# Kernel optimization log

Hardware: AMD Instinct MI355X
Metric: run time of the kernel (lower is better)

Reference implementation:

```python
import jax, jax.numpy as jnp
import numpy as np

B, T, D, W, H = 64, 512, 768, 255, 8
DH = D // H

def layernorm(x, g, b, eps=1e-5):
    m = jnp.mean(x, axis=-1, keepdims=True)
    v = jnp.mean((x - m) ** 2, axis=-1, keepdims=True)
    return (x - m) * jax.lax.rsqrt(v + eps) * g + b

def setup_inputs() -> dict:
    key = jax.random.key(0)
    ks = list(jax.random.split(key, 12))
    p = lambda k, shape, s=0.02: (jax.random.normal(k, shape, jnp.float32) * s)
    # words_ids: -100 at CLS/SEP, each word spans 2 subtokens -> 255 words/row
    wi = np.full((B, T), -100, dtype=np.int32)
    pos = np.arange(1, T - 1)
    wi[:, 1:T - 1] = (pos - 1) // 2
    return {
        'output_bert': jax.random.normal(ks[0], (B, T, D), jnp.float32),
        'words_ids': jnp.asarray(wi),
        'Wq': p(ks[1], (D, D)), 'bq': jnp.zeros((D,), jnp.float32),
        'Wk': p(ks[2], (D, D)), 'bk': jnp.zeros((D,), jnp.float32),
        'Wv': p(ks[3], (D, D)), 'bv': jnp.zeros((D,), jnp.float32),
        'Wo': p(ks[4], (D, D)), 'bo': jnp.zeros((D,), jnp.float32),
        'ln1_g': jnp.ones((D,), jnp.float32), 'ln1_b': jnp.zeros((D,), jnp.float32),
        'W1f': p(ks[5], (D, 4 * D)), 'b1f': jnp.zeros((4 * D,), jnp.float32),
        'W2f': p(ks[6], (4 * D, D)), 'b2f': jnp.zeros((D,), jnp.float32),
        'ln2_g': jnp.ones((D,), jnp.float32), 'ln2_b': jnp.zeros((D,), jnp.float32),
        'ng': jnp.ones((D,), jnp.float32), 'nb': jnp.zeros((D,), jnp.float32),
        'lin_w': p(ks[7], (D, 2)), 'lin_b': jnp.zeros((2,), jnp.float32),
    }

def reference(output_bert, words_ids, Wq, bq, Wk, bk, Wv, bv, Wo, bo,
              ln1_g, ln1_b, W1f, b1f, W2f, b2f, ln2_g, ln2_b, ng, nb, lin_w, lin_b):
    Bsz = output_bert.shape[0]
    # --- first-subtoken gather: first token position of each word id ---
    hits = words_ids[:, None, :] == jnp.arange(W)[None, :, None]   # [B, W, T]
    first_idx = jnp.argmax(hits, axis=-1)                           # [B, W]
    feat = jnp.take_along_axis(output_bert, first_idx[..., None], axis=1)  # [B, W, D]
    # --- transformer encoder layer (post-norm, relu FFN) ---
    q = (feat @ Wq + bq).reshape(Bsz, W, H, DH)
    k = (feat @ Wk + bk).reshape(Bsz, W, H, DH)
    v = (feat @ Wv + bv).reshape(Bsz, W, H, DH)
    scores = jnp.einsum('bqhd,bkhd->bhqk', q, k) * (1.0 / np.sqrt(DH))
    attn = jax.nn.softmax(scores, axis=-1)
    ctx = jnp.einsum('bhqk,bkhd->bqhd', attn, v).reshape(Bsz, W, D)
    x = layernorm(feat + ctx @ Wo + bo, ln1_g, ln1_b)
    ff = jax.nn.relu(x @ W1f + b1f) @ W2f + b2f
    x = layernorm(x + ff, ln2_g, ln2_b)
    # --- final LayerNorm + Linear + softmax + argmax path ---
    x = layernorm(x, ng, nb)
    logits = x @ lin_w + lin_b
    ner_prob = jax.nn.softmax(logits, axis=-1)
    path = jnp.argmax(ner_prob, axis=-1)
    return ner_prob, path
```

## Files before the change

### kernel.cpp

```cpp
#include <hip/hip_runtime.h>
#include <cmath>

#define Bsz 64
#define Tt  512
#define Dd  768
#define Wn  255
#define Hh  8
#define DHd 96
#define NROWS (Bsz*Wn)

typedef _Float16 half_t;
typedef _Float16 f16x8 __attribute__((ext_vector_type(8)));
typedef _Float16 f16x4 __attribute__((ext_vector_type(4)));
typedef float f32x4 __attribute__((ext_vector_type(4)));

#define OFF_QKV 0
#define OFF_WO  5308416
#define OFF_W1  7077888
#define OFF_W2  14155776
#define SLOTH 25165824
__device__ __align__(16) half_t g_w16[21233664];

__device__ __forceinline__ void gload16(const half_t* g, half_t* l) {
    __builtin_amdgcn_global_load_lds((const __attribute__((address_space(1))) void*)g,
                                     (__attribute__((address_space(3))) void*)l, 16, 0, 0);
}


__global__ void k_init_fi(int* fi) {
    int i = blockIdx.x * 256 + threadIdx.x;
    if (i < Bsz * Wn) fi[i] = 0x7fffffff;
}

__global__ void k_scan(const int* __restrict__ wid, int* __restrict__ fi) {
    int i = blockIdx.x * 256 + threadIdx.x;
    if (i >= Bsz * Tt) return;
    int b = i / Tt, t = i % Tt;
    int w = wid[i];
    if (w >= 0 && w < Wn) atomicMin(&fi[b * Wn + w], t);
}

__global__ void k_bcat(const float* __restrict__ bq, const float* __restrict__ bk,
                       const float* __restrict__ bv, float* __restrict__ o) {
    int i = blockIdx.x * 256 + threadIdx.x;
    if (i < 768) o[i] = bq[i];
    else if (i < 1536) o[i] = bk[i - 768];
    else if (i < 2304) o[i] = bv[i - 1536];
}

__global__ void k_gather(const float4* __restrict__ ob, const int* __restrict__ fi,
                         half_t* __restrict__ f16) {
    int i = blockIdx.x * 256 + threadIdx.x;
    if (i >= NROWS * 192) return;
    int r = i / 192, c = i % 192;
    int b = r / Wn;
    int idx = fi[r];
    if (idx == 0x7fffffff) idx = 0;
    float4 v = ob[((size_t)b * Tt + idx) * 192 + c];
    float a0 = v.x * 16.f, a1 = v.y * 16.f, a2 = v.z * 16.f, a3 = v.w * 16.f;
    half_t h0 = (half_t)a0, h1 = (half_t)a1, h2 = (half_t)a2, h3 = (half_t)a3;
    f16x4 hv = {h0, h1, h2, h3};
    f16x4 lv = {(half_t)(a0 - (float)h0), (half_t)(a1 - (float)h1),
                (half_t)(a2 - (float)h2), (half_t)(a3 - (float)h3)};
    size_t off = (size_t)r * 1536 + c * 4;
    *(f16x4*)&f16[off] = hv;
    *(f16x4*)&f16[off + 768] = lv;
}


__global__ void k_wsplit(const float* __restrict__ Wm, int K, int N,
                         size_t obase, int Kseg, size_t cstride) {
    __shared__ float sm[32][33];
    const int tx = threadIdx.x, ty = threadIdx.y;
    const int n0 = blockIdx.x * 32, k0 = blockIdx.y * 32;
    #pragma unroll
    for (int r = 0; r < 4; ++r)
        sm[ty + r * 8][tx] = Wm[(size_t)(k0 + ty + r * 8) * N + n0 + tx];
    __syncthreads();
    #pragma unroll
    for (int r = 0; r < 4; ++r) {
        float v = 64.f * sm[tx][ty + r * 8];
        half_t hi = (half_t)v;
        half_t lo = (half_t)(v - (float)hi);
        int k = k0 + tx;
        int n = n0 + ty + r * 8;
        int c = k / Kseg, kk = k - c * Kseg;
        half_t* o = g_w16 + obase + (size_t)c * cstride + (size_t)n * (3 * Kseg) + kk;
        o[0] = hi; o[Kseg] = hi; o[2 * Kseg] = lo;
    }
}


__device__ __forceinline__ void stage_b(const half_t* B, int Kp3, int col0,
                                        int t, int c, half_t* dst, int tid) {
    int gc = col0 + c * 64 + (tid >> 3);
    int sj = (tid & 7) ^ ((tid >> 3) & 7);
    gload16(B + (size_t)gc * Kp3 + (size_t)t * 64 + sj * 8,
            dst + 16384 + c * 4096 + (tid >> 6) * 512);
}

__device__ __forceinline__ void stage_a0(const half_t* Ap, int lda, int row0, int M,
                                         int kk, int c, half_t* dst, int tid) {
    int gr = row0 + c * 64 + (tid >> 3); if (gr > M - 1) gr = M - 1;
    int sj = (tid & 7) ^ ((tid >> 3) & 7);
    gload16(Ap + (size_t)gr * lda + kk + sj * 8, dst + c * 4096 + (tid >> 6) * 512);
}

__device__ __forceinline__ void stage_a1(const half_t* qcb, int row0, int M,
                                         int kk, int soff, int c, half_t* dst, int tid) {
    int gr = row0 + c * 64 + (tid >> 3); if (gr > M - 1) gr = M - 1;
    int sj = (tid & 7) ^ ((tid >> 3) & 7);
    int k = kk + sj * 8;
    int h = k / 96, d = k - h * 96;
    int b = gr / 255, wl = gr - b * 255;
    gload16(qcb + ((size_t)(b * 8 + h) * 256 + wl) * 192 + d + soff,
            dst + c * 4096 + (tid >> 6) * 512);
}

template<int MODE, int AMODE>
__global__ __launch_bounds__(512, 2) void k_gemm256(
    const half_t* __restrict__ Ah, const half_t* __restrict__ Al, int lda,
    size_t boff, const float* __restrict__ bias,
    const void* res, void* out0, void* out1,
    int M, int N, int K) {
    __shared__ half_t sm[2][32768];
    const int tid = threadIdx.x;
    const int w = tid >> 6, l = tid & 63;
    const int wm = w >> 2, wn = w & 3;
    const int fr = l & 15, q4 = l >> 4;
    const int ck0 = (q4 * 8) ^ ((fr & 7) << 3);
    const int ck1 = ck0 ^ 32;
    const half_t* Bsrc = g_w16 + boff;
    const int Kp3 = 3 * K, NT = Kp3 >> 6;

    int lin = blockIdx.y * gridDim.x + blockIdx.x;
    int nwg = gridDim.x * gridDim.y;
    int wg = (lin & 7) * (nwg >> 3) + (lin >> 3);
    int by = wg / gridDim.x, bx = wg - by * gridDim.x;
    const int row0 = by * 256, col0 = bx * 256;

    f32x4 acc[8][4];
    #pragma unroll
    for (int m = 0; m < 8; ++m)
        #pragma unroll
        for (int n = 0; n < 4; ++n) acc[m][n] = (f32x4){0.f, 0.f, 0.f, 0.f};

    {
        half_t* d0 = &sm[0][0];
        stage_b(Bsrc, Kp3, col0, 0, 0, d0, tid);
        stage_b(Bsrc, Kp3, col0, 0, 1, d0, tid);
        stage_b(Bsrc, Kp3, col0, 0, 2, d0, tid);
        stage_b(Bsrc, Kp3, col0, 0, 3, d0, tid);
        if (AMODE == 0) {
            stage_a0(Ah, lda, row0, M, 0, 0, d0, tid);
            stage_a0(Ah, lda, row0, M, 0, 2, d0, tid);
            stage_a0(Ah, lda, row0, M, 0, 1, d0, tid);
            stage_a0(Ah, lda, row0, M, 0, 3, d0, tid);
        } else {
            stage_a1(Ah, row0, M, 0, 0, 0, d0, tid);
            stage_a1(Ah, row0, M, 0, 0, 2, d0, tid);
            stage_a1(Ah, row0, M, 0, 0, 1, d0, tid);
            stage_a1(Ah, row0, M, 0, 0, 3, d0, tid);
        }
    }
    asm volatile("s_waitcnt vmcnt(2)" ::: "memory");
    __builtin_amdgcn_s_barrier();
    asm volatile("" ::: "memory");

    for (int t = 0; t < NT; ++t) {
        const int p = t & 1;
        half_t* nxtb = &sm[p ^ 1][0];
        const half_t* pA = &sm[p][0] + wm * 8192;
        const half_t* pB = &sm[p][0] + 16384 + wn * 4096;
        const bool pf = (t + 1) < NT;
        const int kn = (t + 1) << 6;
        const int seg = (kn >= 2 * K) ? 2 : ((kn >= K) ? 1 : 0);
        const int kkn = kn - seg * K;
        const half_t* An = (seg == 1) ? Al : Ah;
        const int soff = (seg == 1) ? 96 : 0;

        f16x8 b0[4], b1[4], a0[4], a1[4];
        #pragma unroll
        for (int n = 0; n < 4; ++n) {
            b0[n] = *(const f16x8*)&pB[n * 1024 + fr * 64 + ck0];
            b1[n] = *(const f16x8*)&pB[n * 1024 + fr * 64 + ck1];
        }
        #pragma unroll
        for (int m = 0; m < 4; ++m) {
            a0[m] = *(const f16x8*)&pA[m * 1024 + fr * 64 + ck0];
            a1[m] = *(const f16x8*)&pA[m * 1024 + fr * 64 + ck1];
        }
        if (pf) {
            stage_b(Bsrc, Kp3, col0, t + 1, 0, nxtb, tid);
            stage_b(Bsrc, Kp3, col0, t + 1, 1, nxtb, tid);
            stage_b(Bsrc, Kp3, col0, t + 1, 2, nxtb, tid);
            stage_b(Bsrc, Kp3, col0, t + 1, 3, nxtb, tid);
        }
        __builtin_amdgcn_s_setprio(1);
        #pragma unroll
        for (int m = 0; m < 4; ++m)
            #pragma unroll
            for (int n = 0; n < 4; ++n) {
                acc[m][n] = __builtin_amdgcn_mfma_f32_16x16x32_f16(a0[m], b0[n], acc[m][n], 0, 0, 0);
                acc[m][n] = __builtin_amdgcn_mfma_f32_16x16x32_f16(a1[m], b1[n], acc[m][n], 0, 0, 0);
            }
        __builtin_amdgcn_s_setprio(0);
        if (pf) asm volatile("s_waitcnt vmcnt(4)" ::: "memory");
        else    asm volatile("s_waitcnt vmcnt(0)" ::: "memory");
        __builtin_amdgcn_s_barrier();
        asm volatile("" ::: "memory");

        #pragma unroll
        for (int m = 0; m < 4; ++m) {
            a0[m] = *(const f16x8*)&pA[4096 + m * 1024 + fr * 64 + ck0];
            a1[m] = *(const f16x8*)&pA[4096 + m * 1024 + fr * 64 + ck1];
        }
        if (pf) {
            if (AMODE == 0) {
                stage_a0(An, lda, row0, M, kkn, 0, nxtb, tid);
                stage_a0(An, lda, row0, M, kkn, 2, nxtb, tid);
                stage_a0(An, lda, row0, M, kkn, 1, nxtb, tid);
                stage_a0(An, lda, row0, M, kkn, 3, nxtb, tid);
            } else {
                stage_a1(Ah, row0, M, kkn, soff, 0, nxtb, tid);
                stage_a1(Ah, row0, M, kkn, soff, 2, nxtb, tid);
                stage_a1(Ah, row0, M, kkn, soff, 1, nxtb, tid);
                stage_a1(Ah, row0, M, kkn, soff, 3, nxtb, tid);
            }
        }
        __builtin_amdgcn_s_setprio(1);
        #pragma unroll
        for (int m = 0; m < 4; ++m)
            #pragma unroll
            for (int n = 0; n < 4; ++n) {
                acc[4 + m][n] = __builtin_amdgcn_mfma_f32_16x16x32_f16(a0[m], b0[n], acc[4 + m][n], 0, 0, 0);
                acc[4 + m][n] = __builtin_amdgcn_mfma_f32_16x16x32_f16(a1[m], b1[n], acc[4 + m][n], 0, 0, 0);
            }
        __builtin_amdgcn_s_setprio(0);
        if (pf) {
            asm volatile("s_waitcnt vmcnt(2)" ::: "memory");
            __builtin_amdgcn_s_barrier();
            asm volatile("" ::: "memory");
        }
    }

    const float dsc = 1.0f / 1024.0f;
    #pragma unroll
    for (int m = 0; m < 8; ++m) {
        #pragma unroll
        for (int r = 0; r < 4; ++r) {
            const int row = row0 + wm * 128 + m * 16 + q4 * 4 + r;
            if (row >= M) continue;
            #pragma unroll
            for (int n = 0; n < 4; ++n) {
                const int col = col0 + wn * 64 + n * 16 + fr;
                float vv = acc[m][n][r] * dsc;
                if (MODE != 4) vv += bias[col];
                if (MODE == 5) {
                    int part = col / 768, cc = col - part * 768;
                    int h = cc / 96, d = cc - h * 96;
                    int b = row / 255, wl = row - b * 255;
                    float t16 = vv * 16.f;
                    half_t hi = (half_t)t16;
                    half_t lo = (half_t)(t16 - (float)hi);
                    half_t* dstp = (half_t*)out0 + (size_t)part * SLOTH;
                    size_t o = ((size_t)(b * 8 + h) * 256 + wl) * 192 + d;
                    dstp[o] = hi; dstp[o + 96] = lo;
                } else if (MODE == 1) {
                    const half_t* rp = (const half_t*)res;
                    vv += ((float)rp[(size_t)row * 1536 + col] +
                           (float)rp[(size_t)row * 1536 + 768 + col]) * 0.0625f;
                    ((float*)out0)[(size_t)row * N + col] = vv;
                } else if (MODE == 2) {
                    vv = fmaxf(vv, 0.f);
                    float t16 = vv * 16.f;
                    half_t hi = (half_t)t16;
                    ((half_t*)out0)[(size_t)row * N + col] = hi;
                    ((half_t*)out1)[(size_t)row * N + col] = (half_t)(t16 - (float)hi);
                } else if (MODE == 3) {
                    vv += ((const float*)res)[(size_t)row * N + col];
                    ((float*)out0)[(size_t)row * N + col] = vv;
                } else {
                    float* op = (float*)out0 + (size_t)row * N + col;
                    *op += vv;
                }
            }
        }
    }
}


__global__ __launch_bounds__(256, 2) void k_attn2(half_t* __restrict__ qc,
                                                  const half_t* __restrict__ kk16,
                                                  const half_t* __restrict__ vv16) {
    __shared__ half_t sK[64][200];
    __shared__ half_t sVT[192][72];
    __shared__ float  sP[4][16][68];
    const int tid = threadIdx.x;
    const int w = tid >> 6, l = tid & 63;
    const int lr = l & 15, lc = l >> 4;
    const size_t base = (size_t)blockIdx.x * 49152;
    const float ssc = 0.10206207261596575f / 256.0f;

    for (int pass = 0; pass < 2; ++pass) {
        f32x4 O[2][6];
        float mrow[2][4], lrow[2][4];
        #pragma unroll
        for (int qs = 0; qs < 2; ++qs) {
            #pragma unroll
            for (int dn = 0; dn < 6; ++dn) O[qs][dn] = (f32x4){0.f, 0.f, 0.f, 0.f};
            #pragma unroll
            for (int r = 0; r < 4; ++r) { mrow[qs][r] = -3e38f; lrow[qs][r] = 0.f; }
        }
        for (int kt = 0; kt < 4; ++kt) {
            __syncthreads();
            #pragma unroll
            for (int c = 0; c < 6; ++c) {
                int ch = w + c * 4;
                *(f16x8*)&sK[l][ch * 8] =
                    *(const f16x8*)(kk16 + base + (size_t)(kt * 64 + l) * 192 + ch * 8);
            }
            #pragma unroll
            for (int c = 0; c < 6; ++c) {
                int ch = w + c * 4;
                f16x8 vv = *(const f16x8*)(vv16 + base + (size_t)(kt * 64 + l) * 192 + ch * 8);
                #pragma unroll
                for (int j = 0; j < 8; ++j) sVT[ch * 8 + j][l] = vv[j];
            }
            __syncthreads();
            #pragma unroll
            for (int qs = 0; qs < 2; ++qs) {
                const int qrow0 = (pass * 2 + qs) * 64 + w * 16;
                f16x8 qf0[3], qf1[3];
                #pragma unroll
                for (int s = 0; s < 3; ++s) {
                    qf0[s] = *(const f16x8*)(qc + base + (size_t)(qrow0 + lr) * 192 + s * 32 + lc * 8);
                    qf1[s] = *(const f16x8*)(qc + base + (size_t)(qrow0 + lr) * 192 + 96 + s * 32 + lc * 8);
                }
                f32x4 sacc[4];
                #pragma unroll
                for (int nt = 0; nt < 4; ++nt) sacc[nt] = (f32x4){0.f, 0.f, 0.f, 0.f};
                #pragma unroll
                for (int s = 0; s < 3; ++s)
                    #pragma unroll
                    for (int nt = 0; nt < 4; ++nt) {
                        f16x8 kh = *(const f16x8*)&sK[nt * 16 + lr][s * 32 + lc * 8];
                        f16x8 klo = *(const f16x8*)&sK[nt * 16 + lr][96 + s * 32 + lc * 8];
                        sacc[nt] = __builtin_amdgcn_mfma_f32_16x16x32_f16(qf0[s], kh, sacc[nt], 0, 0, 0);
                        sacc[nt] = __builtin_amdgcn_mfma_f32_16x16x32_f16(qf0[s], klo, sacc[nt], 0, 0, 0);
                        sacc[nt] = __builtin_amdgcn_mfma_f32_16x16x32_f16(qf1[s], kh, sacc[nt], 0, 0, 0);
                    }
                float sv[4][4], mx[4] = {-3e38f, -3e38f, -3e38f, -3e38f};
                #pragma unroll
                for (int nt = 0; nt < 4; ++nt) {
                    int key = kt * 64 + nt * 16 + lr;
                    #pragma unroll
                    for (int r = 0; r < 4; ++r) {
                        float s_ = sacc[nt][r] * ssc;
                        if (key >= 255) s_ = -3e38f;
                        sv[nt][r] = s_;
                        mx[r] = fmaxf(mx[r], s_);
                    }
                }
                #pragma unroll
                for (int r = 0; r < 4; ++r) {
                    mx[r] = fmaxf(mx[r], __shfl_xor(mx[r], 1));
                    mx[r] = fmaxf(mx[r], __shfl_xor(mx[r], 2));
                    mx[r] = fmaxf(mx[r], __shfl_xor(mx[r], 4));
                    mx[r] = fmaxf(mx[r], __shfl_xor(mx[r], 8));
                }
                float alpha[4], rsum[4];
                #pragma unroll
                for (int r = 0; r < 4; ++r) {
                    float mn = fmaxf(mrow[qs][r], mx[r]);
                    alpha[r] = __expf(mrow[qs][r] - mn);
                    mrow[qs][r] = mn;
                    rsum[r] = 0.f;
                }
                float pv[4][4];
                #pragma unroll
                for (int nt = 0; nt < 4; ++nt)
                    #pragma unroll
                    for (int r = 0; r < 4; ++r) {
                        float p = __expf(sv[nt][r] - mrow[qs][r]);
                        pv[nt][r] = p;
                        rsum[r] += p;
                    }
                #pragma unroll
                for (int r = 0; r < 4; ++r) {
                    rsum[r] += __shfl_xor(rsum[r], 1);
                    rsum[r] += __shfl_xor(rsum[r], 2);
                    rsum[r] += __shfl_xor(rsum[r], 4);
                    rsum[r] += __shfl_xor(rsum[r], 8);
                    lrow[qs][r] = lrow[qs][r] * alpha[r] + rsum[r];
                }
                #pragma unroll
                for (int dn = 0; dn < 6; ++dn)
                    #pragma unroll
                    for (int r = 0; r < 4; ++r) O[qs][dn][r] *= alpha[r];
                #pragma unroll
                for (int nt = 0; nt < 4; ++nt)
                    #pragma unroll
                    for (int r = 0; r < 4; ++r)
                        sP[w][lc * 4 + r][nt * 16 + lr] = pv[nt][r];
                #pragma unroll
                for (int ks = 0; ks < 2; ++ks) {
                    const float* pp = &sP[w][lr][ks * 32 + lc * 8];
                    f16x8 ph, pl;
                    #pragma unroll
                    for (int j = 0; j < 8; ++j) {
                        float p = pp[j];
                        half_t h_ = (half_t)p;
                        ph[j] = h_;
                        pl[j] = (half_t)(p - (float)h_);
                    }
                    #pragma unroll
                    for (int dn = 0; dn < 6; ++dn) {
                        f16x8 vh = *(const f16x8*)&sVT[dn * 16 + lr][ks * 32 + lc * 8];
                        f16x8 vl = *(const f16x8*)&sVT[96 + dn * 16 + lr][ks * 32 + lc * 8];
                        O[qs][dn] = __builtin_amdgcn_mfma_f32_16x16x32_f16(ph, vh, O[qs][dn], 0, 0, 0);
                        O[qs][dn] = __builtin_amdgcn_mfma_f32_16x16x32_f16(ph, vl, O[qs][dn], 0, 0, 0);
                        O[qs][dn] = __builtin_amdgcn_mfma_f32_16x16x32_f16(pl, vh, O[qs][dn], 0, 0, 0);
                    }
                }
            }
        }
        #pragma unroll
        for (int qs = 0; qs < 2; ++qs) {
            const int qrow0 = (pass * 2 + qs) * 64 + w * 16;
            #pragma unroll
            for (int r = 0; r < 4; ++r) {
                int qrow = qrow0 + lc * 4 + r;
                if (qrow >= Wn) continue;
                float inv = 1.0f / lrow[qs][r];
                #pragma unroll
                for (int dn = 0; dn < 6; ++dn) {
                    float val = O[qs][dn][r] * inv;
                    half_t hi = (half_t)val;
                    half_t lo = (half_t)(val - (float)hi);
                    size_t o = base + (size_t)qrow * 192 + dn * 16 + lr;
                    qc[o] = hi;
                    qc[o + 96] = lo;
                }
            }
        }
    }
}


template<int SPLIT>
__global__ __launch_bounds__(256) void k_ln(const float* __restrict__ X, const float* __restrict__ g,
                                            const float* __restrict__ bt, float* __restrict__ Y,
                                            half_t* __restrict__ Y16) {
    const int r = blockIdx.x, tid = threadIdx.x;
    __shared__ float red[256];
    const float* x = X + (size_t)r * Dd;
    float x0 = x[tid], x1 = x[tid + 256], x2 = x[tid + 512];
    red[tid] = x0 + x1 + x2; __syncthreads();
    for (int s = 128; s > 0; s >>= 1) { if (tid < s) red[tid] += red[tid + s]; __syncthreads(); }
    float mean = red[0] * (1.0f / 768.0f);
    __syncthreads();
    float d0 = x0 - mean, d1 = x1 - mean, d2 = x2 - mean;
    red[tid] = d0 * d0 + d1 * d1 + d2 * d2; __syncthreads();
    for (int s = 128; s > 0; s >>= 1) { if (tid < s) red[tid] += red[tid + s]; __syncthreads(); }
    float rs = rsqrtf(red[0] * (1.0f / 768.0f) + 1e-5f);
    float* y = Y + (size_t)r * Dd;
    float y0 = d0 * rs * g[tid]       + bt[tid];
    float y1 = d1 * rs * g[tid + 256] + bt[tid + 256];
    float y2 = d2 * rs * g[tid + 512] + bt[tid + 512];
    y[tid] = y0; y[tid + 256] = y1; y[tid + 512] = y2;
    if (SPLIT) {
        half_t* h = Y16 + (size_t)r * 1536;
        float t0 = y0 * 16.f, t1 = y1 * 16.f, t2 = y2 * 16.f;
        half_t h0 = (half_t)t0, h1 = (half_t)t1, h2 = (half_t)t2;
        h[tid] = h0; h[tid + 256] = h1; h[tid + 512] = h2;
        h[768 + tid] = (half_t)(t0 - (float)h0);
        h[768 + tid + 256] = (half_t)(t1 - (float)h1);
        h[768 + tid + 512] = (half_t)(t2 - (float)h2);
    }
}


__global__ __launch_bounds__(256) void k_final(const float* __restrict__ X, const float* __restrict__ g,
                                               const float* __restrict__ bt, const float* __restrict__ lw,
                                               const float* __restrict__ lb, float* __restrict__ out) {
    const int r = blockIdx.x, tid = threadIdx.x;
    __shared__ float red[256];
    const float* x = X + (size_t)r * Dd;
    float x0 = x[tid], x1 = x[tid + 256], x2 = x[tid + 512];
    red[tid] = x0 + x1 + x2; __syncthreads();
    for (int s = 128; s > 0; s >>= 1) { if (tid < s) red[tid] += red[tid + s]; __syncthreads(); }
    float mean = red[0] * (1.0f / 768.0f);
    __syncthreads();
    float d0 = x0 - mean, d1 = x1 - mean, d2 = x2 - mean;
    red[tid] = d0 * d0 + d1 * d1 + d2 * d2; __syncthreads();
    for (int s = 128; s > 0; s >>= 1) { if (tid < s) red[tid] += red[tid + s]; __syncthreads(); }
    float rs = rsqrtf(red[0] * (1.0f / 768.0f) + 1e-5f);
    __syncthreads();
    float n0 = d0 * rs * g[tid]       + bt[tid];
    float n1 = d1 * rs * g[tid + 256] + bt[tid + 256];
    float n2 = d2 * rs * g[tid + 512] + bt[tid + 512];
    float l0 = n0 * lw[2 * tid]     + n1 * lw[2 * (tid + 256)]     + n2 * lw[2 * (tid + 512)];
    float l1 = n0 * lw[2 * tid + 1] + n1 * lw[2 * (tid + 256) + 1] + n2 * lw[2 * (tid + 512) + 1];
    red[tid] = l0; __syncthreads();
    for (int s = 128; s > 0; s >>= 1) { if (tid < s) red[tid] += red[tid + s]; __syncthreads(); }
    l0 = red[0]; __syncthreads();
    red[tid] = l1; __syncthreads();
    for (int s = 128; s > 0; s >>= 1) { if (tid < s) red[tid] += red[tid + s]; __syncthreads(); }
    l1 = red[0];
    if (tid == 0) {
        l0 += lb[0]; l1 += lb[1];
        float m = fmaxf(l0, l1);
        float e0 = expf(l0 - m), e1 = expf(l1 - m);
        float inv = 1.0f / (e0 + e1);
        out[2 * r] = e0 * inv;
        out[2 * r + 1] = e1 * inv;
        out[2 * NROWS + r] = (l1 > l0) ? 1.0f : 0.0f;
    }
}


extern "C" void kernel_launch(void* const* d_in, const int* in_sizes, int n_in,
                              void* d_out, int out_size, void* d_ws, size_t ws_size,
                              hipStream_t stream) {
    const float* ob  = (const float*)d_in[0];
    const int*   wid = (const int*)d_in[1];
    const float* Wq  = (const float*)d_in[2];  const float* bq  = (const float*)d_in[3];
    const float* Wk  = (const float*)d_in[4];  const float* bk  = (const float*)d_in[5];
    const float* Wv  = (const float*)d_in[6];  const float* bv  = (const float*)d_in[7];
    const float* Wo  = (const float*)d_in[8];  const float* bo  = (const float*)d_in[9];
    const float* g1  = (const float*)d_in[10]; const float* b1  = (const float*)d_in[11];
    const float* W1f = (const float*)d_in[12]; const float* b1f = (const float*)d_in[13];
    const float* W2f = (const float*)d_in[14]; const float* b2f = (const float*)d_in[15];
    const float* g2  = (const float*)d_in[16]; const float* b2  = (const float*)d_in[17];
    const float* ng  = (const float*)d_in[18]; const float* nb  = (const float*)d_in[19];
    const float* lw  = (const float*)d_in[20]; const float* lb  = (const float*)d_in[21];
    float* out = (float*)d_out;

    char* ws = (char*)d_ws;
    const size_t MB = 1u << 20;
    const size_t SLOT = 48 * MB;
    int* fi = (int*)ws;
    float* bcat = (float*)(ws + 262144);
    char* S1 = ws + MB;
    char* S2 = S1 + SLOT;
    char* S3 = S2 + SLOT;
    char* S4 = S3 + SLOT;

    half_t* feat16 = (half_t*)S1;
    half_t* q16    = (half_t*)S2;
    half_t* k16    = (half_t*)S3;
    half_t* v16    = (half_t*)S4;
    float*  t1     = (float*)S3;
    float*  xbuf   = (float*)S4;
    half_t* x16    = (half_t*)S2;
    half_t* ffh_h  = (half_t*)S1;
    half_t* ffh_l  = (half_t*)S3;
    float*  x2     = (float*)S2;

    k_wsplit<<<dim3(24, 24), dim3(32, 8), 0, stream>>>(Wq, 768, 768, OFF_QKV,                   768, 0);
    k_wsplit<<<dim3(24, 24), dim3(32, 8), 0, stream>>>(Wk, 768, 768, OFF_QKV + 768ul * 2304,    768, 0);
    k_wsplit<<<dim3(24, 24), dim3(32, 8), 0, stream>>>(Wv, 768, 768, OFF_QKV + 1536ul * 2304,   768, 0);
    k_wsplit<<<dim3(24, 24), dim3(32, 8), 0, stream>>>(Wo, 768, 768, OFF_WO,                    768, 0);
    k_wsplit<<<dim3(96, 24), dim3(32, 8), 0, stream>>>(W1f, 768, 3072, OFF_W1,                  768, 0);
    k_wsplit<<<dim3(24, 96), dim3(32, 8), 0, stream>>>(W2f, 3072, 768, OFF_W2,                 1024, 768ul * 3072);
    k_bcat<<<9, 256, 0, stream>>>(bq, bk, bv, bcat);

    k_init_fi<<<(Bsz * Wn + 255) / 256, 256, 0, stream>>>(fi);
    k_scan<<<(Bsz * Tt) / 256, 256, 0, stream>>>(wid, fi);
    k_gather<<<(NROWS * 192 + 255) / 256, 256, 0, stream>>>((const float4*)ob, fi, feat16);

    k_gemm256<5, 0><<<dim3(9, 64), 512, 0, stream>>>(
        feat16, feat16 + 768, 1536, OFF_QKV, bcat, nullptr, q16, nullptr, NROWS, 2304, 768);

    k_attn2<<<Bsz * Hh, 256, 0, stream>>>(q16, k16, v16);

    k_gemm256<1, 1><<<dim3(3, 64), 512, 0, stream>>>(
        q16, q16 + 96, 0, OFF_WO, bo, feat16, t1, nullptr, NROWS, 768, 768);
    k_ln<1><<<NROWS, 256, 0, stream>>>(t1, g1, b1, xbuf, x16);

    for (int c = 0; c < 3; ++c) {
        k_gemm256<2, 0><<<dim3(4, 64), 512, 0, stream>>>(
            x16, x16 + 768, 1536, OFF_W1 + (size_t)c * 1024 * 2304, b1f + c * 1024,
            nullptr, ffh_h, ffh_l, NROWS, 1024, 768);
        if (c == 0)
            k_gemm256<3, 0><<<dim3(3, 64), 512, 0, stream>>>(
                ffh_h, ffh_l, 1024, OFF_W2, b2f, xbuf, xbuf, nullptr, NROWS, 768, 1024);
        else
            k_gemm256<4, 0><<<dim3(3, 64), 512, 0, stream>>>(
                ffh_h, ffh_l, 1024, OFF_W2 + (size_t)c * 768 * 3072, b2f,
                nullptr, xbuf, nullptr, NROWS, 768, 1024);
    }

    k_ln<0><<<NROWS, 256, 0, stream>>>(xbuf, g2, b2, x2, nullptr);
    k_final<<<NROWS, 256, 0, stream>>>(x2, ng, nb, lw, lb, out);
}
```

Before: 1.206 ms.

## Shrink GEMM tiles to 128x192 for higher occupancy and re-chunk FFN by 768

Replaces the 256x256-tile split-fp16 GEMM with a 128x192 tile using less LDS, so four workgroups fit per CU instead of two, and restructures the K-loop staging so B is staged in three 64-column chunks. The FFN is now processed in four 768-wide chunks instead of three 1024-wide chunks, and W2 is re-split with a matching stride. The aim is more workgroups in flight and better CU fill on the 16320-row problem. The cost is lower data reuse per tile, meaning more global and LDS traffic per FLOP, plus extra kernel launches.

```diff
diff --git a/kernel.cpp b/kernel.cpp
--- a/kernel.cpp
+++ b/kernel.cpp
@@ -18,12 +18,20 @@
 #define OFF_WO  5308416
 #define OFF_W1  7077888
 #define OFF_W2  14155776
+#define W2_CSTR 1769472
 #define SLOTH 25165824
 __device__ __align__(16) half_t g_w16[21233664];
 
 __device__ __forceinline__ void gload16(const half_t* g, half_t* l) {
     __builtin_amdgcn_global_load_lds((const __attribute__((address_space(1))) void*)g,
                                      (__attribute__((address_space(3))) void*)l, 16, 0, 0);
+}
+
+template<int N> __device__ __forceinline__ void waitv() {
+    if constexpr (N == 0) asm volatile("s_waitcnt vmcnt(0)" ::: "memory");
+    else if constexpr (N == 1) asm volatile("s_waitcnt vmcnt(1)" ::: "memory");
+    else if constexpr (N == 2) asm volatile("s_waitcnt vmcnt(2)" ::: "memory");
+    else if constexpr (N == 4) asm volatile("s_waitcnt vmcnt(4)" ::: "memory");
 }
 
 
@@ -96,7 +104,7 @@
     int gc = col0 + c * 64 + (tid >> 3);
     int sj = (tid & 7) ^ ((tid >> 3) & 7);
     gload16(B + (size_t)gc * Kp3 + (size_t)t * 64 + sj * 8,
-            dst + 16384 + c * 4096 + (tid >> 6) * 512);
+            dst + 8192 + c * 4096 + (tid >> 6) * 512);
 }
 
 __device__ __forceinline__ void stage_a0(const half_t* Ap, int lda, int row0, int M,
@@ -118,12 +126,12 @@
 }
 
 template<int MODE, int AMODE>
-__global__ __launch_bounds__(512, 2) void k_gemm256(
+__global__ __launch_bounds__(512, 4) void k_gemm128(
     const half_t* __restrict__ Ah, const half_t* __restrict__ Al, int lda,
     size_t boff, const float* __restrict__ bias,
     const void* res, void* out0, void* out1,
     int M, int N, int K) {
-    __shared__ half_t sm[2][32768];
+    __shared__ half_t sm[2][20480];
     const int tid = threadIdx.x;
     const int w = tid >> 6, l = tid & 63;
     const int wm = w >> 2, wn = w & 3;
@@ -137,41 +145,36 @@
     int nwg = gridDim.x * gridDim.y;
     int wg = (lin & 7) * (nwg >> 3) + (lin >> 3);
     int by = wg / gridDim.x, bx = wg - by * gridDim.x;
-    const int row0 = by * 256, col0 = bx * 256;
-
-    f32x4 acc[8][4];
+    const int row0 = by * 128, col0 = bx * 192;
+
+    f32x4 acc[4][3];
     #pragma unroll
-    for (int m = 0; m < 8; ++m)
-        #pragma unroll
-        for (int n = 0; n < 4; ++n) acc[m][n] = (f32x4){0.f, 0.f, 0.f, 0.f};
+    for (int m = 0; m < 4; ++m)
+        #pragma unroll
+        for (int j = 0; j < 3; ++j) acc[m][j] = (f32x4){0.f, 0.f, 0.f, 0.f};
 
     {
         half_t* d0 = &sm[0][0];
         stage_b(Bsrc, Kp3, col0, 0, 0, d0, tid);
         stage_b(Bsrc, Kp3, col0, 0, 1, d0, tid);
-        stage_b(Bsrc, Kp3, col0, 0, 2, d0, tid);
-        stage_b(Bsrc, Kp3, col0, 0, 3, d0, tid);
         if (AMODE == 0) {
             stage_a0(Ah, lda, row0, M, 0, 0, d0, tid);
-            stage_a0(Ah, lda, row0, M, 0, 2, d0, tid);
             stage_a0(Ah, lda, row0, M, 0, 1, d0, tid);
-            stage_a0(Ah, lda, row0, M, 0, 3, d0, tid);
         } else {
             stage_a1(Ah, row0, M, 0, 0, 0, d0, tid);
-            stage_a1(Ah, row0, M, 0, 0, 2, d0, tid);
             stage_a1(Ah, row0, M, 0, 0, 1, d0, tid);
-            stage_a1(Ah, row0, M, 0, 0, 3, d0, tid);
-        }
-    }
-    asm volatile("s_waitcnt vmcnt(2)" ::: "memory");
+        }
+        stage_b(Bsrc, Kp3, col0, 0, 2, d0, tid);
+    }
+    waitv<1>();
     __builtin_amdgcn_s_barrier();
     asm volatile("" ::: "memory");
 
     for (int t = 0; t < NT; ++t) {
         const int p = t & 1;
         half_t* nxtb = &sm[p ^ 1][0];
-        const half_t* pA = &sm[p][0] + wm * 8192;
-        const half_t* pB = &sm[p][0] + 16384 + wn * 4096;
+        const half_t* pA = &sm[p][0] + wm * 4096;
+        const half_t* pB = &sm[p][8192];
         const bool pf = (t + 1) < NT;
         const int kn = (t + 1) << 6;
         const int seg = (kn >= 2 * K) ? 2 : ((kn >= K) ? 1 : 0);
@@ -179,11 +182,12 @@
         const half_t* An = (seg == 1) ? Al : Ah;
         const int soff = (seg == 1) ? 96 : 0;
 
-        f16x8 b0[4], b1[4], a0[4], a1[4];
-        #pragma unroll
-        for (int n = 0; n < 4; ++n) {
-            b0[n] = *(const f16x8*)&pB[n * 1024 + fr * 64 + ck0];
-            b1[n] = *(const f16x8*)&pB[n * 1024 + fr * 64 + ck1];
+        f16x8 b0[2], b1[2], a0[4], a1[4];
+        #pragma unroll
+        for (int j = 0; j < 2; ++j) {
+            const half_t* p_ = &pB[j * 4096 + (wn * 16 + fr) * 64];
+            b0[j] = *(const f16x8*)&p_[ck0];
+            b1[j] = *(const f16x8*)&p_[ck1];
         }
         #pragma unroll
         for (int m = 0; m < 4; ++m) {
@@ -193,52 +197,44 @@
         if (pf) {
             stage_b(Bsrc, Kp3, col0, t + 1, 0, nxtb, tid);
             stage_b(Bsrc, Kp3, col0, t + 1, 1, nxtb, tid);
-            stage_b(Bsrc, Kp3, col0, t + 1, 2, nxtb, tid);
-            stage_b(Bsrc, Kp3, col0, t + 1, 3, nxtb, tid);
+            if (AMODE == 0) {
+                stage_a0(An, lda, row0, M, kkn, 0, nxtb, tid);
+                stage_a0(An, lda, row0, M, kkn, 1, nxtb, tid);
+            } else {
+                stage_a1(Ah, row0, M, kkn, soff, 0, nxtb, tid);
+                stage_a1(Ah, row0, M, kkn, soff, 1, nxtb, tid);
+            }
         }
         __builtin_amdgcn_s_setprio(1);
         #pragma unroll
         for (int m = 0; m < 4; ++m)
             #pragma unroll
-            for (int n = 0; n < 4; ++n) {
-                acc[m][n] = __builtin_amdgcn_mfma_f32_16x16x32_f16(a0[m], b0[n], acc[m][n], 0, 0, 0);
-                acc[m][n] = __builtin_amdgcn_mfma_f32_16x16x32_f16(a1[m], b1[n], acc[m][n], 0, 0, 0);
+            for (int j = 0; j < 2; ++j) {
+                acc[m][j] = __builtin_amdgcn_mfma_f32_16x16x32_f16(a0[m], b0[j], acc[m][j], 0, 0, 0);
+                acc[m][j] = __builtin_amdgcn_mfma_f32_16x16x32_f16(a1[m], b1[j], acc[m][j], 0, 0, 0);
             }
         __builtin_amdgcn_s_setprio(0);
-        if (pf) asm volatile("s_waitcnt vmcnt(4)" ::: "memory");
-        else    asm volatile("s_waitcnt vmcnt(0)" ::: "memory");
+        if (pf) waitv<4>();
+        else    waitv<0>();
         __builtin_amdgcn_s_barrier();
         asm volatile("" ::: "memory");
 
+        f16x8 c0, c1;
+        {
+            const half_t* p_ = &pB[2 * 4096 + (wn * 16 + fr) * 64];
+            c0 = *(const f16x8*)&p_[ck0];
+            c1 = *(const f16x8*)&p_[ck1];
+        }
+        if (pf) stage_b(Bsrc, Kp3, col0, t + 1, 2, nxtb, tid);
+        __builtin_amdgcn_s_setprio(1);
         #pragma unroll
         for (int m = 0; m < 4; ++m) {
-            a0[m] = *(const f16x8*)&pA[4096 + m * 1024 + fr * 64 + ck0];
-            a1[m] = *(const f16x8*)&pA[4096 + m * 1024 + fr * 64 + ck1];
-        }
-        if (pf) {
-            if (AMODE == 0) {
-                stage_a0(An, lda, row0, M, kkn, 0, nxtb, tid);
-                stage_a0(An, lda, row0, M, kkn, 2, nxtb, tid);
-                stage_a0(An, lda, row0, M, kkn, 1, nxtb, tid);
-                stage_a0(An, lda, row0, M, kkn, 3, nxtb, tid);
-            } else {
-                stage_a1(Ah, row0, M, kkn, soff, 0, nxtb, tid);
-                stage_a1(Ah, row0, M, kkn, soff, 2, nxtb, tid);
-                stage_a1(Ah, row0, M, kkn, soff, 1, nxtb, tid);
-                stage_a1(Ah, row0, M, kkn, soff, 3, nxtb, tid);
-            }
-        }
-        __builtin_amdgcn_s_setprio(1);
-        #pragma unroll
-        for (int m = 0; m < 4; ++m)
-            #pragma unroll
-            for (int n = 0; n < 4; ++n) {
-                acc[4 + m][n] = __builtin_amdgcn_mfma_f32_16x16x32_f16(a0[m], b0[n], acc[4 + m][n], 0, 0, 0);
-                acc[4 + m][n] = __builtin_amdgcn_mfma_f32_16x16x32_f16(a1[m], b1[n], acc[4 + m][n], 0, 0, 0);
-            }
+            acc[m][2] = __builtin_amdgcn_mfma_f32_16x16x32_f16(a0[m], c0, acc[m][2], 0, 0, 0);
+            acc[m][2] = __builtin_amdgcn_mfma_f32_16x16x32_f16(a1[m], c1, acc[m][2], 0, 0, 0);
+        }
         __builtin_amdgcn_s_setprio(0);
         if (pf) {
-            asm volatile("s_waitcnt vmcnt(2)" ::: "memory");
+            waitv<1>();
             __builtin_amdgcn_s_barrier();
             asm volatile("" ::: "memory");
         }
@@ -246,15 +242,15 @@
 
     const float dsc = 1.0f / 1024.0f;
     #pragma unroll
-    for (int m = 0; m < 8; ++m) {
+    for (int m = 0; m < 4; ++m) {
         #pragma unroll
         for (int r = 0; r < 4; ++r) {
-            const int row = row0 + wm * 128 + m * 16 + q4 * 4 + r;
+            const int row = row0 + wm * 64 + m * 16 + q4 * 4 + r;
             if (row >= M) continue;
             #pragma unroll
-            for (int n = 0; n < 4; ++n) {
-                const int col = col0 + wn * 64 + n * 16 + fr;
-                float vv = acc[m][n][r] * dsc;
+            for (int j = 0; j < 3; ++j) {
+                const int col = col0 + j * 64 + wn * 16 + fr;
+                float vv = acc[m][j][r] * dsc;
                 if (MODE != 4) vv += bias[col];
                 if (MODE == 5) {
                     int part = col / 768, cc = col - part * 768;
@@ -563,33 +559,33 @@
     k_wsplit<<<dim3(24, 24), dim3(32, 8), 0, stream>>>(Wv, 768, 768, OFF_QKV + 1536ul * 2304,   768, 0);
     k_wsplit<<<dim3(24, 24), dim3(32, 8), 0, stream>>>(Wo, 768, 768, OFF_WO,                    768, 0);
     k_wsplit<<<dim3(96, 24), dim3(32, 8), 0, stream>>>(W1f, 768, 3072, OFF_W1,                  768, 0);
-    k_wsplit<<<dim3(24, 96), dim3(32, 8), 0, stream>>>(W2f, 3072, 768, OFF_W2,                 1024, 768ul * 3072);
+    k_wsplit<<<dim3(24, 96), dim3(32, 8), 0, stream>>>(W2f, 3072, 768, OFF_W2,                  768, W2_CSTR);
     k_bcat<<<9, 256, 0, stream>>>(bq, bk, bv, bcat);
 
     k_init_fi<<<(Bsz * Wn + 255) / 256, 256, 0, stream>>>(fi);
     k_scan<<<(Bsz * Tt) / 256, 256, 0, stream>>>(wid, fi);
     k_gather<<<(NROWS * 192 + 255) / 256, 256, 0, stream>>>((const float4*)ob, fi, feat16);
 
-    k_gemm256<5, 0><<<dim3(9, 64), 512, 0, stream>>>(
+    k_gemm128<5, 0><<<dim3(12, 128), 512, 0, stream>>>(
         feat16, feat16 + 768, 1536, OFF_QKV, bcat, nullptr, q16, nullptr, NROWS, 2304, 768);
 
     k_attn2<<<Bsz * Hh, 256, 0, stream>>>(q16, k16, v16);
 
-    k_gemm256<1, 1><<<dim3(3, 64), 512, 0, stream>>>(
+    k_gemm128<1, 1><<<dim3(4, 128), 512, 0, stream>>>(
         q16, q16 + 96, 0, OFF_WO, bo, feat16, t1, nullptr, NROWS, 768, 768);
     k_ln<1><<<NROWS, 256, 0, stream>>>(t1, g1, b1, xbuf, x16);
 
-    for (int c = 0; c < 3; ++c) {
-        k_gemm256<2, 0><<<dim3(4, 64), 512, 0, stream>>>(
-            x16, x16 + 768, 1536, OFF_W1 + (size_t)c * 1024 * 2304, b1f + c * 1024,
-            nullptr, ffh_h, ffh_l, NROWS, 1024, 768);
+    for (int c = 0; c < 4; ++c) {
+        k_gemm128<2, 0><<<dim3(4, 128), 512, 0, stream>>>(
+            x16, x16 + 768, 1536, OFF_W1 + (size_t)c * 768 * 2304, b1f + c * 768,
+            nullptr, ffh_h, ffh_l, NROWS, 768, 768);
         if (c == 0)
-            k_gemm256<3, 0><<<dim3(3, 64), 512, 0, stream>>>(
-                ffh_h, ffh_l, 1024, OFF_W2, b2f, xbuf, xbuf, nullptr, NROWS, 768, 1024);
+            k_gemm128<3, 0><<<dim3(4, 128), 512, 0, stream>>>(
+                ffh_h, ffh_l, 768, OFF_W2, b2f, xbuf, xbuf, nullptr, NROWS, 768, 768);
         else
-            k_gemm256<4, 0><<<dim3(3, 64), 512, 0, stream>>>(
-                ffh_h, ffh_l, 1024, OFF_W2 + (size_t)c * 768 * 3072, b2f,
-                nullptr, xbuf, nullptr, NROWS, 768, 1024);
+            k_gemm128<4, 0><<<dim3(4, 128), 512, 0, stream>>>(
+                ffh_h, ffh_l, 768, OFF_W2 + (size_t)c * W2_CSTR, b2f,
+                nullptr, xbuf, nullptr, NROWS, 768, 768);
     }
 
     k_ln<0><<<NROWS, 256, 0, stream>>>(xbuf, g2, b2, x2, nullptr);
```

After: 1.163 ms. 1.04x faster.
